# Kernel tuning notes

Measured on AMD Instinct MI355X. Metric: run time of the kernel, lower is better.

Reference implementation:

```python
import jax, jax.numpy as jnp
import numpy as np

B, S, D = 2, 2048, 1024
H, HD = 16, 64  # num_heads, hidden_size per head


def setup_inputs() -> dict:
    key = jax.random.key(0)
    ks = jax.random.split(key, 10)
    inp = {
        'queries': jax.random.normal(ks[0], (B, S, D), jnp.float32),
        'keys': jax.random.normal(ks[1], (B, S, D), jnp.float32),
        'values': jax.random.normal(ks[2], (B, S, D), jnp.float32),
        # binary indicator masks (some zeros so renorm guard path is exercised)
        'ind_q': (jax.random.uniform(ks[3], (B, S)) > 0.2).astype(jnp.float32),
        'ind_k': (jax.random.uniform(ks[4], (B, S)) > 0.2).astype(jnp.float32),
        'ind_v': (jax.random.uniform(ks[5], (B, S)) > 0.2).astype(jnp.float32),
        'Wq': jax.random.normal(ks[6], (D, H * HD), jnp.float32) / np.sqrt(D),
        'Wk': jax.random.normal(ks[7], (D, H * HD), jnp.float32) / np.sqrt(D),
        'Wv': jax.random.normal(ks[8], (D, H * HD), jnp.float32) / np.sqrt(D),
        'Wo': jax.random.normal(ks[9], (H * HD, D), jnp.float32) / np.sqrt(H * HD),
    }
    return inp


def reference(queries, keys, values, ind_q, ind_k, ind_v, Wq, Wk, Wv, Wo):
    b, nq, _ = queries.shape
    nk = keys.shape[1]
    # projections -> [B, H, S, HD], masked by indicators
    Q = (queries @ Wq).reshape(b, nq, H, HD).transpose(0, 2, 1, 3) * ind_q[:, None, :, None]
    K = (keys @ Wk).reshape(b, nk, H, HD).transpose(0, 2, 1, 3) * ind_k[:, None, :, None]
    V = (values @ Wv).reshape(b, nk, H, HD).transpose(0, 2, 1, 3) * ind_v[:, None, :, None]
    # scaled dot-product scores, plain softmax over keys
    scores = jnp.einsum('bhqd,bhkd->bhqk', Q, K) / jnp.sqrt(jnp.float32(HD))
    attn = jax.nn.softmax(scores, axis=-1)
    # post-softmax multiplicative key-indicator mask + renormalization with zero-row guard
    attn = attn * ind_k[:, None, None, :]
    denom = jnp.sum(attn, axis=-1, keepdims=True)
    attn = attn / jnp.where(denom == 0.0, 1.0, denom)
    out = jnp.einsum('bhqk,bhkd->bhqd', attn, V)  # [B, H, Q, HD]
    out = out.transpose(0, 2, 1, 3).reshape(b, nq, H * HD)
    return out @ Wo
```

## Files before the change

### kernel.cpp

```cpp
#include <hip/hip_runtime.h>
#include <math.h>

typedef __attribute__((ext_vector_type(8))) short bf16x8;
typedef __attribute__((ext_vector_type(4))) float f32x4;

__device__ __forceinline__ unsigned short f2b(float f) {
    union { float f; unsigned int u; } v; v.f = f;
    unsigned int u = v.u + 0x7FFFu + ((v.u >> 16) & 1u);
    return (unsigned short)(u >> 16);
}

__device__ __forceinline__ f32x4 mfma16(bf16x8 a, bf16x8 b, f32x4 c) {
    return __builtin_amdgcn_mfma_f32_16x16x32_bf16(a, b, c, 0, 0, 0);
}

__device__ __forceinline__ void async_ld16(void* l, const void* g) {
    __builtin_amdgcn_global_load_lds(
        (__attribute__((address_space(1))) void*)g,
        (__attribute__((address_space(3))) void*)l, 16, 0, 0);
}

__device__ __forceinline__ float exp2_hw(float x) {
    float r; asm("v_exp_f32 %0, %1" : "=v"(r) : "v"(x)); return r;
}

__device__ __forceinline__ unsigned int cvtpk_bf16(float a, float b) {
    unsigned int r;
    asm("v_cvt_pk_bf16_f32 %0, %1, %2" : "=v"(r) : "v"(a), "v"(b));
    return r;
}

__global__ __launch_bounds__(256) void cvt_tr(
    const float* __restrict__ W0, const float* __restrict__ W1,
    const float* __restrict__ W2, const float* __restrict__ W3,
    unsigned short* __restrict__ T0, unsigned short* __restrict__ T1,
    unsigned short* __restrict__ T2, unsigned short* __restrict__ T3)
{
    const int z = blockIdx.z;
    const float* W = (z == 0) ? W0 : (z == 1) ? W1 : (z == 2) ? W2 : W3;
    unsigned short* T = (z == 0) ? T0 : (z == 1) ? T1 : (z == 2) ? T2 : T3;
    __shared__ short Ls[64 * 65];
    const int t = threadIdx.x;
    const int k0 = blockIdx.x * 64, n0 = blockIdx.y * 64;
#pragma unroll
    for (int ii = 0; ii < 4; ++ii) {
        const int kl = (t >> 4) + 16 * ii, nl = (t & 15) * 4;
        const float4 v = *(const float4*)&W[(size_t)(k0 + kl) * 1024 + n0 + nl];
        Ls[kl * 65 + nl + 0] = (short)f2b(v.x);
        Ls[kl * 65 + nl + 1] = (short)f2b(v.y);
        Ls[kl * 65 + nl + 2] = (short)f2b(v.z);
        Ls[kl * 65 + nl + 3] = (short)f2b(v.w);
    }
    __syncthreads();
#pragma unroll
    for (int ii = 0; ii < 4; ++ii) {
        const int nl = (t >> 4) + 16 * ii, kl = (t & 15) * 4;
        ushort4 o;
        o.x = (unsigned short)Ls[(kl + 0) * 65 + nl];
        o.y = (unsigned short)Ls[(kl + 1) * 65 + nl];
        o.z = (unsigned short)Ls[(kl + 2) * 65 + nl];
        o.w = (unsigned short)Ls[(kl + 3) * 65 + nl];
        *(ushort4*)&T[(size_t)(n0 + nl) * 1024 + k0 + kl] = o;
    }
}

__global__ __launch_bounds__(256) void gemm_proj3(
    const float* __restrict__ qf, const float* __restrict__ kf,
    const float* __restrict__ vf,
    const unsigned short* __restrict__ Wqt, const unsigned short* __restrict__ Wkt,
    const unsigned short* __restrict__ Wvt,
    unsigned short* __restrict__ Qw, unsigned short* __restrict__ Kw,
    unsigned short* __restrict__ Vw,
    const float* __restrict__ iq, const float* __restrict__ ik,
    const float* __restrict__ iv)
{
    const unsigned hw = blockIdx.x;
    const unsigned xcd = hw & 7, j = hw >> 3;
    const unsigned panel = xcd * 12 + (j >> 3);
    const unsigned nt = j & 7;
    const int z = panel >> 5, mt = panel & 31;

    const float* A           = (z == 0) ? qf  : (z == 1) ? kf  : vf;
    const unsigned short* Bt = (z == 0) ? Wqt : (z == 1) ? Wkt : Wvt;
    unsigned short* Cw       = (z == 0) ? Qw  : (z == 1) ? Kw  : Vw;
    const float* msk         = (z == 0) ? iq  : (z == 1) ? ik  : iv;
    const float scale = (z == 0) ? 0.125f * 1.44269504088896f : 1.0f;

    __shared__ __align__(16) short As[2][128 * 32];
    __shared__ __align__(16) short Bs[2][128 * 32];
    __shared__ float maskL[128];
    const int t = threadIdx.x;
    const int w = t >> 6, lane = t & 63, l15 = lane & 15, quad = lane >> 4;
    const int wr = w >> 1, wc = w & 1;
    const int n0 = nt * 128, m0 = mt * 128;
    if (t < 128) maskL[t] = msk[m0 + t] * scale;

    const int ar = t >> 1, ac = (t & 1) * 16;
    const float* Arow          = A  + (size_t)(m0 + ar) * 1024 + ac;
    const unsigned short* Brow = Bt + (size_t)(n0 + ar) * 1024 + ac;

    float4 a4[4];
    bf16x8 b8[2];
    a4[0] = *(const float4*)(Arow + 0);
    a4[1] = *(const float4*)(Arow + 4);
    a4[2] = *(const float4*)(Arow + 8);
    a4[3] = *(const float4*)(Arow + 12);
    b8[0] = *(const bf16x8*)(Brow + 0);
    b8[1] = *(const bf16x8*)(Brow + 8);

    f32x4 zero4 = {0.f, 0.f, 0.f, 0.f};
    f32x4 acc[4][4];
#pragma unroll
    for (int i = 0; i < 4; ++i)
#pragma unroll
        for (int j2 = 0; j2 < 4; ++j2) acc[i][j2] = zero4;

    for (int step = 0; step < 32; ++step) {
        const int cur = step & 1;
        {
            uint4 lo, hi;
            lo.x = cvtpk_bf16(a4[0].x, a4[0].y); lo.y = cvtpk_bf16(a4[0].z, a4[0].w);
            lo.z = cvtpk_bf16(a4[1].x, a4[1].y); lo.w = cvtpk_bf16(a4[1].z, a4[1].w);
            hi.x = cvtpk_bf16(a4[2].x, a4[2].y); hi.y = cvtpk_bf16(a4[2].z, a4[2].w);
            hi.z = cvtpk_bf16(a4[3].x, a4[3].y); hi.w = cvtpk_bf16(a4[3].z, a4[3].w);
            *(uint4*)&As[cur][ar * 32 + ac]     = lo;
            *(uint4*)&As[cur][ar * 32 + ac + 8] = hi;
            *(bf16x8*)&Bs[cur][ar * 32 + ac]     = b8[0];
            *(bf16x8*)&Bs[cur][ar * 32 + ac + 8] = b8[1];
        }
        __syncthreads();
        {
            const int kn = (step < 31 ? step + 1 : 31) * 32;
            a4[0] = *(const float4*)(Arow + kn + 0);
            a4[1] = *(const float4*)(Arow + kn + 4);
            a4[2] = *(const float4*)(Arow + kn + 8);
            a4[3] = *(const float4*)(Arow + kn + 12);
            b8[0] = *(const bf16x8*)(Brow + kn + 0);
            b8[1] = *(const bf16x8*)(Brow + kn + 8);
        }
        bf16x8 af[4], bfr[4];
#pragma unroll
        for (int i = 0; i < 4; ++i)
            af[i] = *(const bf16x8*)&As[cur][(64 * wr + 16 * i + l15) * 32 + 8 * quad];
#pragma unroll
        for (int j2 = 0; j2 < 4; ++j2)
            bfr[j2] = *(const bf16x8*)&Bs[cur][(64 * wc + 16 * j2 + l15) * 32 + 8 * quad];
        __builtin_amdgcn_s_setprio(1);
#pragma unroll
        for (int i = 0; i < 4; ++i)
#pragma unroll
            for (int j2 = 0; j2 < 4; ++j2)
                acc[i][j2] = mfma16(af[i], bfr[j2], acc[i][j2]);
        __builtin_amdgcn_s_setprio(0);
    }

    const int h = 2 * nt + wc;
#pragma unroll
    for (int i = 0; i < 4; ++i)
#pragma unroll
        for (int j2 = 0; j2 < 4; ++j2)
#pragma unroll
            for (int reg = 0; reg < 4; ++reg) {
                const int mloc = 64 * wr + 16 * i + 4 * quad + reg;
                const int m = m0 + mloc;
                const int bb = m >> 11, s = m & 2047;
                const int hd = 16 * j2 + l15;
                Cw[((size_t)(bb * 16 + h) * 2048 + s) * 64 + hd] =
                    f2b(acc[i][j2][reg] * maskL[mloc]);
            }
}

__global__ __launch_bounds__(256) void gemm_out(
    const unsigned short* __restrict__ A, const unsigned short* __restrict__ Bt,
    float* __restrict__ C)
{
    __shared__ __align__(16) short As[128 * 32];
    __shared__ __align__(16) short Bs[64 * 32];
    const int t = threadIdx.x;
    const int w = t >> 6, lane = t & 63, l15 = lane & 15, quad = lane >> 4;
    const int wr = w >> 1, wc = w & 1;
    const unsigned hw = blockIdx.x;
    const unsigned xcd = hw & 7, j = hw >> 3;
    const unsigned mt = xcd * 4 + (j >> 4);
    const unsigned nt = j & 15;
    const int n0 = nt * 64, m0 = mt * 128;
    const int srow = lane >> 2, soff = (lane & 3) * 8;

    f32x4 zero4 = {0.f, 0.f, 0.f, 0.f};
    f32x4 acc[4][2];
#pragma unroll
    for (int i = 0; i < 4; ++i) { acc[i][0] = zero4; acc[i][1] = zero4; }

    for (int k0 = 0; k0 < 1024; k0 += 32) {
        __syncthreads();
#pragma unroll
        for (int i = 0; i < 2; ++i) {
            const int r = 16 * (2 * w + i);
            async_ld16(As + r * 32, A + (size_t)(m0 + r + srow) * 1024 + k0 + soff);
        }
        async_ld16(Bs + (16 * w) * 32, Bt + (size_t)(n0 + 16 * w + srow) * 1024 + k0 + soff);
        __syncthreads();
        bf16x8 af[4], bfr[2];
#pragma unroll
        for (int i = 0; i < 4; ++i)
            af[i] = *(const bf16x8*)&As[(64 * wr + 16 * i + l15) * 32 + 8 * quad];
#pragma unroll
        for (int jj = 0; jj < 2; ++jj)
            bfr[jj] = *(const bf16x8*)&Bs[(32 * wc + 16 * jj + l15) * 32 + 8 * quad];
#pragma unroll
        for (int i = 0; i < 4; ++i)
#pragma unroll
            for (int jj = 0; jj < 2; ++jj)
                acc[i][jj] = mfma16(af[i], bfr[jj], acc[i][jj]);
    }
#pragma unroll
    for (int i = 0; i < 4; ++i)
#pragma unroll
        for (int jj = 0; jj < 2; ++jj)
#pragma unroll
            for (int reg = 0; reg < 4; ++reg) {
                const int m = m0 + 64 * wr + 16 * i + 4 * quad + reg;
                const int n = n0 + 32 * wc + 16 * jj + l15;
                C[(size_t)m * 1024 + n] = acc[i][jj][reg];
            }
}

#define GST 72

__global__ __launch_bounds__(512, 4) void attn_mfma(
    const unsigned short* __restrict__ Qw, const unsigned short* __restrict__ Kw,
    const unsigned short* __restrict__ Vw, const float* __restrict__ indk,
    unsigned short* __restrict__ AO)
{
    __shared__ __align__(16) short Ks[2][64 * GST];
    __shared__ __align__(16) short Vt[2][64 * GST];
    __shared__ float Bl[2048];
    const int t = threadIdx.x;
    const int w = t >> 6, lane = t & 63, l15 = lane & 15, quad = lane >> 4;
    const unsigned wg = (blockIdx.x & 7) * 64 + (blockIdx.x >> 3);
    const int q0 = (wg & 15) * 128;
    const int h = (wg >> 4) & 15, b = wg >> 8;
    const size_t base = (size_t)(b * 16 + h) * (2048 * 64);
    const unsigned short* Qb = Qw + base + (size_t)q0 * 64;
    const unsigned short* Kb = Kw + base;
    const unsigned short* Vb = Vw + base;

    bf16x8 qf[2];
    qf[0] = *(const bf16x8*)&Qb[(16 * w + l15) * 64 + 8 * quad];
    qf[1] = *(const bf16x8*)&Qb[(16 * w + l15) * 64 + 32 + 8 * quad];

    {
        const float4 bi = *(const float4*)&indk[b * 2048 + t * 4];
        float4 bo;
        bo.x = (bi.x - 1.f) * 1e30f; bo.y = (bi.y - 1.f) * 1e30f;
        bo.z = (bi.z - 1.f) * 1e30f; bo.w = (bi.w - 1.f) * 1e30f;
        *(float4*)&Bl[t * 4] = bo;
    }

    const int skr = t >> 3, skc = (t & 7) * 8;
    const int slr = skr ^ (((skr >> 3) & 1) << 2);
    const int dq = t >> 5, kp2 = (t & 31) * 2;

    bf16x8 kreg;
    ushort4 vreg[2];
    kreg = *(const bf16x8*)&Kb[(size_t)skr * 64 + skc];
    vreg[0] = *(const ushort4*)&Vb[(size_t)kp2 * 64 + 4 * dq];
    vreg[1] = *(const ushort4*)&Vb[(size_t)(kp2 + 1) * 64 + 4 * dq];

    const int u_ = l15 >> 2, a_ = l15 & 3;
    const int krA = 8 * u_ + 4 * (u_ & 1) + a_;
    const int krB = 8 * u_ + 4 * (1 - (u_ & 1)) + a_;

    f32x4 zero4 = {0.f, 0.f, 0.f, 0.f};
    f32x4 oacc[4];
    oacc[0] = zero4; oacc[1] = zero4; oacc[2] = zero4; oacc[3] = zero4;
    float l_part = 0.f;

    for (int c = 0; c < 32; ++c) {
        const int cur = c & 1;
        *(bf16x8*)&Ks[cur][slr * GST + skc] = kreg;
        {
            const unsigned int* v0d = (const unsigned int*)&vreg[0];
            const unsigned int* v1d = (const unsigned int*)&vreg[1];
            *(unsigned int*)&Vt[cur][(4 * dq + 0) * GST + kp2] =
                __builtin_amdgcn_perm(v1d[0], v0d[0], 0x05040100u);
            *(unsigned int*)&Vt[cur][(4 * dq + 1) * GST + kp2] =
                __builtin_amdgcn_perm(v1d[0], v0d[0], 0x07060302u);
            *(unsigned int*)&Vt[cur][(4 * dq + 2) * GST + kp2] =
                __builtin_amdgcn_perm(v1d[1], v0d[1], 0x05040100u);
            *(unsigned int*)&Vt[cur][(4 * dq + 3) * GST + kp2] =
                __builtin_amdgcn_perm(v1d[1], v0d[1], 0x07060302u);
        }
        __syncthreads();
        {
            const int kn = (c < 31 ? c + 1 : 31) * 64;
            kreg = *(const bf16x8*)&Kb[(size_t)(kn + skr) * 64 + skc];
            vreg[0] = *(const ushort4*)&Vb[(size_t)(kn + kp2) * 64 + 4 * dq];
            vreg[1] = *(const ushort4*)&Vb[(size_t)(kn + kp2 + 1) * 64 + 4 * dq];
        }
        const short* KsC = Ks[cur];
        const short* VtC = Vt[cur];
        const float* BlC = Bl + c * 64;

        f32x4 sacc[4];
#pragma unroll
        for (int g = 0; g < 4; ++g) {
            const float4 bv = *(const float4*)&BlC[32 * (g >> 1) + 4 * (g & 1) + 8 * quad];
            sacc[g][0] = bv.x; sacc[g][1] = bv.y; sacc[g][2] = bv.z; sacc[g][3] = bv.w;
        }
        __builtin_amdgcn_s_setprio(1);
#pragma unroll
        for (int ks = 0; ks < 2; ++ks)
#pragma unroll
            for (int g = 0; g < 4; ++g) {
                const int row = 32 * (g >> 1) + ((g & 1) ? krB : krA);
                const bf16x8 kf = *(const bf16x8*)&KsC[row * GST + 32 * ks + 8 * quad];
                sacc[g] = mfma16(kf, qf[ks], sacc[g]);
            }
        __builtin_amdgcn_s_setprio(0);

        unsigned int dw[4][2];
#pragma unroll
        for (int g = 0; g < 4; ++g) {
#pragma unroll
            for (int r = 0; r < 4; ++r) sacc[g][r] = exp2_hw(sacc[g][r]);
            dw[g][0] = cvtpk_bf16(sacc[g][0], sacc[g][1]);
            dw[g][1] = cvtpk_bf16(sacc[g][2], sacc[g][3]);
        }

        __builtin_amdgcn_s_setprio(1);
#pragma unroll
        for (int ks = 0; ks < 2; ++ks) {
            union { unsigned int u[4]; bf16x8 b; } pc;
            pc.u[0] = dw[2 * ks][0];     pc.u[1] = dw[2 * ks][1];
            pc.u[2] = dw[2 * ks + 1][0]; pc.u[3] = dw[2 * ks + 1][1];
#pragma unroll
            for (int nj = 0; nj < 4; ++nj) {
                const bf16x8 vbf = *(const bf16x8*)
                    &VtC[(16 * nj + l15) * GST + 32 * ks + 8 * quad];
                oacc[nj] = mfma16(pc.b, vbf, oacc[nj]);
            }
        }
        __builtin_amdgcn_s_setprio(0);

        float rg[4];
#pragma unroll
        for (int g = 0; g < 4; ++g)
            rg[g] = (sacc[g][0] + sacc[g][1]) + (sacc[g][2] + sacc[g][3]);
        l_part += (rg[0] + rg[1]) + (rg[2] + rg[3]);
    }

    float l = l_part;
    l += __shfl_xor(l, 16);
    l += __shfl_xor(l, 32);
    const float inv = (l > 0.f) ? 1.f / l : 0.f;
    float invr[4];
#pragma unroll
    for (int r = 0; r < 4; ++r) invr[r] = __shfl(inv, 4 * quad + r);
#pragma unroll
    for (int nj = 0; nj < 4; ++nj)
#pragma unroll
        for (int r = 0; r < 4; ++r) {
            const int row = q0 + 16 * w + 4 * quad + r;
            AO[(size_t)(b * 2048 + row) * 1024 + h * 64 + 16 * nj + l15] =
                f2b(oacc[nj][r] * invr[r]);
        }
}

extern "C" void kernel_launch(void* const* d_in, const int* in_sizes, int n_in,
                              void* d_out, int out_size, void* d_ws, size_t ws_size,
                              hipStream_t stream) {
    const float* q  = (const float*)d_in[0];
    const float* k  = (const float*)d_in[1];
    const float* v  = (const float*)d_in[2];
    const float* iq = (const float*)d_in[3];
    const float* ik = (const float*)d_in[4];
    const float* iv = (const float*)d_in[5];
    const float* Wq = (const float*)d_in[6];
    const float* Wk = (const float*)d_in[7];
    const float* Wv = (const float*)d_in[8];
    const float* Wo = (const float*)d_in[9];
    float* out = (float*)d_out;
    unsigned short* ws = (unsigned short*)d_ws;

    const size_t M1 = 1048576;
    unsigned short* Wqt = ws + 12 * M1;
    unsigned short* Wkt = ws + 13 * M1;
    unsigned short* Wvt = ws + 14 * M1;
    unsigned short* Wot = ws + 15 * M1;
    unsigned short* Qw  = ws + 16 * M1;
    unsigned short* Kw  = ws + 20 * M1;
    unsigned short* Vw  = ws + 24 * M1;
    unsigned short* AO  = ws + 28 * M1;

    cvt_tr<<<dim3(16, 16, 4), dim3(256), 0, stream>>>(Wq, Wk, Wv, Wo, Wqt, Wkt, Wvt, Wot);
    gemm_proj3<<<dim3(768, 1, 1), dim3(256), 0, stream>>>(
        q, k, v, Wqt, Wkt, Wvt, Qw, Kw, Vw, iq, ik, iv);
    attn_mfma<<<dim3(512, 1, 1), dim3(512), 0, stream>>>(Qw, Kw, Vw, ik, AO);
    gemm_out<<<dim3(512, 1, 1), dim3(256), 0, stream>>>(AO, Wot, out);
}
```

Measured before the change: 225.4 us.

## Deepen register prefetch to two stages in projection and output GEMMs

Measured after the change: 228.5 us. No clear change (+1.3%).

```diff
diff --git a/kernel.cpp b/kernel.cpp
--- a/kernel.cpp
+++ b/kernel.cpp
@@ -12,12 +12,6 @@
 
 __device__ __forceinline__ f32x4 mfma16(bf16x8 a, bf16x8 b, f32x4 c) {
     return __builtin_amdgcn_mfma_f32_16x16x32_bf16(a, b, c, 0, 0, 0);
-}
-
-__device__ __forceinline__ void async_ld16(void* l, const void* g) {
-    __builtin_amdgcn_global_load_lds(
-        (__attribute__((address_space(1))) void*)g,
-        (__attribute__((address_space(3))) void*)l, 16, 0, 0);
 }
 
 __device__ __forceinline__ float exp2_hw(float x) {
@@ -64,7 +58,7 @@
     }
 }
 
-__global__ __launch_bounds__(256) void gemm_proj3(
+__global__ __launch_bounds__(256, 3) void gemm_proj3(
     const float* __restrict__ qf, const float* __restrict__ kf,
     const float* __restrict__ vf,
     const unsigned short* __restrict__ Wqt, const unsigned short* __restrict__ Wkt,
@@ -99,14 +93,19 @@
     const float* Arow          = A  + (size_t)(m0 + ar) * 1024 + ac;
     const unsigned short* Brow = Bt + (size_t)(n0 + ar) * 1024 + ac;
 
-    float4 a4[4];
-    bf16x8 b8[2];
-    a4[0] = *(const float4*)(Arow + 0);
-    a4[1] = *(const float4*)(Arow + 4);
-    a4[2] = *(const float4*)(Arow + 8);
-    a4[3] = *(const float4*)(Arow + 12);
-    b8[0] = *(const bf16x8*)(Brow + 0);
-    b8[1] = *(const bf16x8*)(Brow + 8);
+#define PLDA(SET, kn) \
+    SET[0] = *(const float4*)(Arow + (kn) + 0); \
+    SET[1] = *(const float4*)(Arow + (kn) + 4); \
+    SET[2] = *(const float4*)(Arow + (kn) + 8); \
+    SET[3] = *(const float4*)(Arow + (kn) + 12);
+#define PLDB(SET, kn) \
+    SET[0] = *(const bf16x8*)(Brow + (kn) + 0); \
+    SET[1] = *(const bf16x8*)(Brow + (kn) + 8);
+
+    float4 aA[4], aB[4];
+    bf16x8 bA[2], bB[2];
+    PLDA(aA, 0)  PLDB(bA, 0)
+    PLDA(aB, 32) PLDB(bB, 32)
 
     f32x4 zero4 = {0.f, 0.f, 0.f, 0.f};
     f32x4 acc[4][4];
@@ -115,44 +114,42 @@
 #pragma unroll
         for (int j2 = 0; j2 < 4; ++j2) acc[i][j2] = zero4;
 
-    for (int step = 0; step < 32; ++step) {
-        const int cur = step & 1;
-        {
-            uint4 lo, hi;
-            lo.x = cvtpk_bf16(a4[0].x, a4[0].y); lo.y = cvtpk_bf16(a4[0].z, a4[0].w);
-            lo.z = cvtpk_bf16(a4[1].x, a4[1].y); lo.w = cvtpk_bf16(a4[1].z, a4[1].w);
-            hi.x = cvtpk_bf16(a4[2].x, a4[2].y); hi.y = cvtpk_bf16(a4[2].z, a4[2].w);
-            hi.z = cvtpk_bf16(a4[3].x, a4[3].y); hi.w = cvtpk_bf16(a4[3].z, a4[3].w);
-            *(uint4*)&As[cur][ar * 32 + ac]     = lo;
-            *(uint4*)&As[cur][ar * 32 + ac + 8] = hi;
-            *(bf16x8*)&Bs[cur][ar * 32 + ac]     = b8[0];
-            *(bf16x8*)&Bs[cur][ar * 32 + ac + 8] = b8[1];
-        }
-        __syncthreads();
-        {
-            const int kn = (step < 31 ? step + 1 : 31) * 32;
-            a4[0] = *(const float4*)(Arow + kn + 0);
-            a4[1] = *(const float4*)(Arow + kn + 4);
-            a4[2] = *(const float4*)(Arow + kn + 8);
-            a4[3] = *(const float4*)(Arow + kn + 12);
-            b8[0] = *(const bf16x8*)(Brow + kn + 0);
-            b8[1] = *(const bf16x8*)(Brow + kn + 8);
-        }
-        bf16x8 af[4], bfr[4];
-#pragma unroll
-        for (int i = 0; i < 4; ++i)
-            af[i] = *(const bf16x8*)&As[cur][(64 * wr + 16 * i + l15) * 32 + 8 * quad];
-#pragma unroll
-        for (int j2 = 0; j2 < 4; ++j2)
-            bfr[j2] = *(const bf16x8*)&Bs[cur][(64 * wc + 16 * j2 + l15) * 32 + 8 * quad];
-        __builtin_amdgcn_s_setprio(1);
-#pragma unroll
-        for (int i = 0; i < 4; ++i)
-#pragma unroll
-            for (int j2 = 0; j2 < 4; ++j2)
-                acc[i][j2] = mfma16(af[i], bfr[j2], acc[i][j2]);
-        __builtin_amdgcn_s_setprio(0);
-    }
+#define PSTEP(ASET, BSET, CUR, cc) { \
+    { uint4 lo, hi; \
+      lo.x = cvtpk_bf16(ASET[0].x, ASET[0].y); lo.y = cvtpk_bf16(ASET[0].z, ASET[0].w); \
+      lo.z = cvtpk_bf16(ASET[1].x, ASET[1].y); lo.w = cvtpk_bf16(ASET[1].z, ASET[1].w); \
+      hi.x = cvtpk_bf16(ASET[2].x, ASET[2].y); hi.y = cvtpk_bf16(ASET[2].z, ASET[2].w); \
+      hi.z = cvtpk_bf16(ASET[3].x, ASET[3].y); hi.w = cvtpk_bf16(ASET[3].z, ASET[3].w); \
+      *(uint4*)&As[CUR][ar * 32 + ac]     = lo; \
+      *(uint4*)&As[CUR][ar * 32 + ac + 8] = hi; \
+      *(bf16x8*)&Bs[CUR][ar * 32 + ac]     = BSET[0]; \
+      *(bf16x8*)&Bs[CUR][ar * 32 + ac + 8] = BSET[1]; } \
+    { const int kn = ((cc) + 2 < 32 ? (cc) + 2 : 31) * 32; \
+      PLDA(ASET, kn) PLDB(BSET, kn) } \
+    __syncthreads(); \
+    { bf16x8 af[4], bfr[4]; \
+      _Pragma("unroll") \
+      for (int i = 0; i < 4; ++i) \
+          af[i] = *(const bf16x8*)&As[CUR][(64 * wr + 16 * i + l15) * 32 + 8 * quad]; \
+      _Pragma("unroll") \
+      for (int j2 = 0; j2 < 4; ++j2) \
+          bfr[j2] = *(const bf16x8*)&Bs[CUR][(64 * wc + 16 * j2 + l15) * 32 + 8 * quad]; \
+      __builtin_amdgcn_s_setprio(1); \
+      _Pragma("unroll") \
+      for (int i = 0; i < 4; ++i) \
+          _Pragma("unroll") \
+          for (int j2 = 0; j2 < 4; ++j2) \
+              acc[i][j2] = mfma16(af[i], bfr[j2], acc[i][j2]); \
+      __builtin_amdgcn_s_setprio(0); } \
+}
+
+    for (int c = 0; c < 32; c += 2) {
+        PSTEP(aA, bA, 0, c)
+        PSTEP(aB, bB, 1, c + 1)
+    }
+#undef PSTEP
+#undef PLDA
+#undef PLDB
 
     const int h = 2 * nt + wc;
 #pragma unroll
@@ -174,8 +171,8 @@
     const unsigned short* __restrict__ A, const unsigned short* __restrict__ Bt,
     float* __restrict__ C)
 {
-    __shared__ __align__(16) short As[128 * 32];
-    __shared__ __align__(16) short Bs[64 * 32];
+    __shared__ __align__(16) short As[2][128 * 32];
+    __shared__ __align__(16) short Bs[2][64 * 32];
     const int t = threadIdx.x;
     const int w = t >> 6, lane = t & 63, l15 = lane & 15, quad = lane >> 4;
     const int wr = w >> 1, wc = w & 1;
@@ -184,35 +181,56 @@
     const unsigned mt = xcd * 4 + (j >> 4);
     const unsigned nt = j & 15;
     const int n0 = nt * 64, m0 = mt * 128;
-    const int srow = lane >> 2, soff = (lane & 3) * 8;
+
+    const int ar = t >> 1, ac = (t & 1) * 16;
+    const int br = t >> 2, bc = (t & 3) * 8;
+    const unsigned short* Arow = A  + (size_t)(m0 + ar) * 1024 + ac;
+    const unsigned short* Brow = Bt + (size_t)(n0 + br) * 1024 + bc;
+
+#define OLD(ASET, BREG, kn) \
+    ASET[0] = *(const bf16x8*)(Arow + (kn) + 0); \
+    ASET[1] = *(const bf16x8*)(Arow + (kn) + 8); \
+    BREG    = *(const bf16x8*)(Brow + (kn));
+
+    bf16x8 aA[2], aB[2], bA, bB;
+    OLD(aA, bA, 0)
+    OLD(aB, bB, 32)
 
     f32x4 zero4 = {0.f, 0.f, 0.f, 0.f};
     f32x4 acc[4][2];
 #pragma unroll
     for (int i = 0; i < 4; ++i) { acc[i][0] = zero4; acc[i][1] = zero4; }
 
-    for (int k0 = 0; k0 < 1024; k0 += 32) {
-        __syncthreads();
-#pragma unroll
-        for (int i = 0; i < 2; ++i) {
-            const int r = 16 * (2 * w + i);
-            async_ld16(As + r * 32, A + (size_t)(m0 + r + srow) * 1024 + k0 + soff);
-        }
-        async_ld16(Bs + (16 * w) * 32, Bt + (size_t)(n0 + 16 * w + srow) * 1024 + k0 + soff);
-        __syncthreads();
-        bf16x8 af[4], bfr[2];
-#pragma unroll
-        for (int i = 0; i < 4; ++i)
-            af[i] = *(const bf16x8*)&As[(64 * wr + 16 * i + l15) * 32 + 8 * quad];
-#pragma unroll
-        for (int jj = 0; jj < 2; ++jj)
-            bfr[jj] = *(const bf16x8*)&Bs[(32 * wc + 16 * jj + l15) * 32 + 8 * quad];
-#pragma unroll
-        for (int i = 0; i < 4; ++i)
-#pragma unroll
-            for (int jj = 0; jj < 2; ++jj)
-                acc[i][jj] = mfma16(af[i], bfr[jj], acc[i][jj]);
-    }
+#define OSTEP(ASET, BREG, CUR, cc) { \
+    *(bf16x8*)&As[CUR][ar * 32 + ac]     = ASET[0]; \
+    *(bf16x8*)&As[CUR][ar * 32 + ac + 8] = ASET[1]; \
+    *(bf16x8*)&Bs[CUR][br * 32 + bc]     = BREG; \
+    { const int kn = ((cc) + 2 < 32 ? (cc) + 2 : 31) * 32; \
+      OLD(ASET, BREG, kn) } \
+    __syncthreads(); \
+    { bf16x8 af[4], bfr[2]; \
+      _Pragma("unroll") \
+      for (int i = 0; i < 4; ++i) \
+          af[i] = *(const bf16x8*)&As[CUR][(64 * wr + 16 * i + l15) * 32 + 8 * quad]; \
+      _Pragma("unroll") \
+      for (int jj = 0; jj < 2; ++jj) \
+          bfr[jj] = *(const bf16x8*)&Bs[CUR][(32 * wc + 16 * jj + l15) * 32 + 8 * quad]; \
+      __builtin_amdgcn_s_setprio(1); \
+      _Pragma("unroll") \
+      for (int i = 0; i < 4; ++i) \
+          _Pragma("unroll") \
+          for (int jj = 0; jj < 2; ++jj) \
+              acc[i][jj] = mfma16(af[i], bfr[jj], acc[i][jj]); \
+      __builtin_amdgcn_s_setprio(0); } \
+}
+
+    for (int c = 0; c < 32; c += 2) {
+        OSTEP(aA, bA, 0, c)
+        OSTEP(aB, bB, 1, c + 1)
+    }
+#undef OSTEP
+#undef OLD
+
 #pragma unroll
     for (int i = 0; i < 4; ++i)
 #pragma unroll
```
